# Kernel tuning notes

Hardware: AMD Instinct MI355X
Metric: run time of the kernel (lower is better)

Reference implementation:

```python
import jax, jax.numpy as jnp
import numpy as np

B, L, C = 16, 4096, 32
D = 512
W = 24                  # rolling window
LAGS = [3, 5, 7]
MAXLEN = 5000
EPS = 1e-5


def setup_inputs() -> dict:
    key = jax.random.key(0)
    ks = jax.random.split(key, 8)
    return {
        "x": jax.random.normal(ks[0], (B, L, C), jnp.float32),
        "conv_w": jax.random.normal(ks[1], (D, C * (5 + len(LAGS)), 3), jnp.float32) * 0.05,
        "conv_b": jnp.zeros((D,), jnp.float32),
        "learned_pe": jax.random.normal(ks[2], (1, MAXLEN, D), jnp.float32) * (1.0 / np.sqrt(D)),
        "tape_pos": jax.random.normal(ks[3], (MAXLEN, D), jnp.float32) * 0.02,
        "tproj_w": jax.random.normal(ks[4], (D, D), jnp.float32) * 0.02,
        "tproj_b": jnp.zeros((D,), jnp.float32),
        "mixer_w": jax.random.normal(ks[5], (D, 2 * D), jnp.float32) * 0.02,
        "mixer_b": jnp.zeros((D,), jnp.float32),
        "g_c": jnp.ones((D,), jnp.float32), "b_c": jnp.zeros((D,), jnp.float32),
        "g_f": jnp.ones((D,), jnp.float32), "b_f": jnp.zeros((D,), jnp.float32),
        "g_l": jnp.ones((D,), jnp.float32), "b_l": jnp.zeros((D,), jnp.float32),
        "g_t": jnp.ones((D,), jnp.float32), "b_t": jnp.zeros((D,), jnp.float32),
        "weight_params": jnp.array([0.25, 0.25, 0.25, 0.25], jnp.float32),
    }


def _layer_norm(h, g, b):
    m = jnp.mean(h, axis=-1, keepdims=True)
    v = jnp.mean((h - m) ** 2, axis=-1, keepdims=True)
    return g * (h - m) / jnp.sqrt(v + EPS) + b


def reference(x, conv_w, conv_b, learned_pe, tape_pos, tproj_w, tproj_b,
              mixer_w, mixer_b, g_c, b_c, g_f, b_f, g_l, b_l, g_t, b_t,
              weight_params):
    Bx, Lx, Cx = x.shape
    # --- RollingFeatureExtractor: replicate-pad left, sliding mean/max/min/std
    xp = jnp.pad(x, ((0, 0), (W - 1, 0), (0, 0)), mode="edge")          # [B, L+W-1, C]
    win = jnp.stack([xp[:, i:i + Lx, :] for i in range(W)], axis=2)       # [B, L, W, C]
    w_mean = jnp.mean(win, axis=2)
    w_max = jnp.max(win, axis=2)
    w_min = jnp.min(win, axis=2)
    w_var = jnp.sum((win - w_mean[:, :, None, :]) ** 2, axis=2) / (W - 1)  # unbiased, torch.std default
    w_std = jnp.sqrt(w_var)
    x_stats = jnp.concatenate([x, w_mean, w_max, w_min, w_std], axis=-1)  # [B, L, 5C]
    # --- lag differences (replicate pad left by max lag)
    ml = max(LAGS)
    xl = jnp.pad(x, ((0, 0), (ml, 0), (0, 0)), mode="edge")
    x_lags = jnp.concatenate([x - xl[:, ml - l:ml - l + Lx, :] for l in LAGS], axis=-1)  # [B, L, 3C]
    comb = jnp.concatenate([x_stats, x_lags], axis=-1)                    # [B, L, 8C]
    # --- TokenEmbedding: Conv1d k=3, circular padding
    h = comb.transpose(0, 2, 1)                                           # [B, 8C, L]
    h = jnp.pad(h, ((0, 0), (0, 0), (1, 1)), mode="wrap")
    h = jax.lax.conv_general_dilated(h, conv_w, (1,), "VALID",
                                     dimension_numbers=("NCH", "OIH", "NCH"))
    h = h + conv_b[None, :, None]
    combined_emb = _layer_norm(h.transpose(0, 2, 1), g_c, b_c)            # [B, L, D]
    # --- fixed sinusoidal PE (constant / detached)
    pos = jnp.arange(Lx)
    div = jnp.exp(jnp.arange(0, D, 2).astype(x.dtype) * (-(np.log(10000.0) / D)))
    ang = pos[:, None].astype(x.dtype) * div[None, :]                     # [L, D/2]
    pe_fixed_tab = jnp.zeros((Lx, D), x.dtype).at[:, 0::2].set(jnp.sin(ang)).at[:, 1::2].set(jnp.cos(ang))
    pe_fixed = _layer_norm(pe_fixed_tab, g_f, b_f)[None]                  # [1, L, D]
    # --- learnable PE
    pe_learned = _layer_norm(learned_pe[:, :Lx], g_l, b_l)                # [1, L, D]
    # --- tAPE: token proj + learned pos embedding -> mixer linear
    pe = tape_pos[pos]                                                    # [L, D]
    tok = combined_emb @ tproj_w.T + tproj_b                              # [B, L, D]
    mixed = jnp.concatenate([tok, jnp.broadcast_to(pe[None], tok.shape)], axis=-1)
    pe_tape = _layer_norm(mixed @ mixer_w.T + mixer_b, g_t, b_t)          # [B, L, D]
    # --- softmax-weighted sum (dropout is identity in eval)
    w = jax.nn.softmax(weight_params)
    return (w[0] * combined_emb + w[1] * pe_fixed + w[2] * pe_learned + w[3] * pe_tape)
```

## Files before the change

### kernel.cpp

```cpp
#include <hip/hip_runtime.h>
#include <stdint.h>


typedef unsigned short u16;
using short8  = __attribute__((ext_vector_type(8))) short;
using floatx4 = __attribute__((ext_vector_type(4))) float;
typedef __attribute__((address_space(1))) const unsigned int u32_as1;
typedef __attribute__((address_space(3))) unsigned int       u32_as3;

static __device__ __forceinline__ u16 f2b(float f) {
  unsigned u = __float_as_uint(f);
  u += 0x7FFFu + ((u >> 16) & 1u);
  return (u16)(u >> 16);
}
static __device__ __forceinline__ float b2f(u16 h) {
  return __uint_as_float(((unsigned)h) << 16);
}

__global__ __launch_bounds__(256) void prep_mats(
    const float* __restrict__ conv_w, const float* __restrict__ mixer_w,
    const float* __restrict__ tproj_w, const float* __restrict__ tape_pos,
    u16* __restrict__ W1, u16* __restrict__ A_m1, u16* __restrict__ M2t,
    u16* __restrict__ tprojT, u16* __restrict__ tape_bf) {
  int i = blockIdx.x * 256 + threadIdx.x;
  if (i < 393216) {
    int d = i / 768, rem = i - d * 768;
    int j = rem >> 8, c = rem & 255;
    W1[i] = f2b(conv_w[(d * 256 + c) * 3 + j]);
  } else if (i < 393216 + 262144) {
    int k = i - 393216; int p = k >> 9, r = k & 511;
    A_m1[k] = f2b(mixer_w[p * 1024 + r]);
  } else if (i < 393216 + 524288) {
    int k = i - 393216 - 262144; int p = k >> 9, r = k & 511;
    M2t[k] = f2b(mixer_w[p * 1024 + 512 + r]);
  } else if (i < 393216 + 786432) {
    int k = i - 393216 - 524288; int q = k >> 9, r = k & 511;
    tprojT[k] = f2b(tproj_w[r * 512 + q]);
  } else if (i < 393216 + 786432 + 2097152) {
    int k = i - 393216 - 786432;
    tape_bf[k] = f2b(tape_pos[k]);
  }
}

__global__ __launch_bounds__(256) void bias2_k(
    const float* __restrict__ mixer_w, const float* __restrict__ tproj_b,
    const float* __restrict__ mixer_b, float* __restrict__ bias2) {
  int p = blockIdx.x * 256 + threadIdx.x;
  if (p < 512) {
    float s = mixer_b[p];
    for (int r = 0; r < 512; ++r) s += mixer_w[p * 1024 + r] * tproj_b[r];
    bias2[p] = s;
  }
}

__global__ __launch_bounds__(256) void feat_kernel(
    const float* __restrict__ x, u16* __restrict__ comb) {
  __shared__ float sx[87 * 32];
  const int b = blockIdx.y, l0 = blockIdx.x * 64;
  for (int idx = threadIdx.x; idx < 87 * 32; idx += 256) {
    int r = idx >> 5, c = idx & 31;
    int ls = l0 - 23 + r; if (ls < 0) ls = 0;
    sx[idx] = x[((size_t)b * 4096 + ls) * 32 + c];
  }
  __syncthreads();
  const int c = threadIdx.x & 31, lr0 = threadIdx.x >> 5;
  for (int pass = 0; pass < 8; ++pass) {
    int lr = pass * 8 + lr0;
    int l = l0 + lr;
    float w[24];
    float s = 0.f, mx = -3.4e38f, mn = 3.4e38f;
    #pragma unroll
    for (int i = 0; i < 24; ++i) {
      float v = sx[(lr + i) * 32 + c];
      w[i] = v; s += v; mx = fmaxf(mx, v); mn = fminf(mn, v);
    }
    float mean = s * (1.f / 24.f);
    float ssd = 0.f;
    #pragma unroll
    for (int i = 0; i < 24; ++i) { float d = w[i] - mean; ssd += d * d; }
    float sd = sqrtf(fmaxf(ssd, 0.f) * (1.f / 23.f));
    float xv = w[23];
    float lag3 = xv - sx[(lr + 20) * 32 + c];
    float lag5 = xv - sx[(lr + 18) * 32 + c];
    float lag7 = xv - sx[(lr + 16) * 32 + c];
    size_t base = ((size_t)b * 4096 + l) * 256 + c;
    comb[base +   0] = f2b(xv);
    comb[base +  32] = f2b(mean);
    comb[base +  64] = f2b(mx);
    comb[base +  96] = f2b(mn);
    comb[base + 128] = f2b(sd);
    comb[base + 160] = f2b(lag3);
    comb[base + 192] = f2b(lag5);
    comb[base + 224] = f2b(lag7);
  }
}

__global__ __launch_bounds__(256) void gemm_bt(
    const u16* __restrict__ A, const u16* __restrict__ Bt,
    void* __restrict__ outp, int K, int ldc,
    const float* __restrict__ bias, int outBf16) {
  __shared__ __align__(16) u16 lA[128 * 64];
  __shared__ __align__(16) u16 lB[128 * 64];
  const int tid = threadIdx.x;
  const int m0 = blockIdx.x * 128, n0 = blockIdx.y * 128;
  const int wave = tid >> 6, lane = tid & 63;
  const int wm = (wave & 1) * 64, wn = (wave >> 1) * 64;
  const int quad = lane >> 4, r16 = lane & 15;
  const int rowT = tid >> 3, col8 = tid & 7;

  floatx4 acc[4][4];
  #pragma unroll
  for (int i = 0; i < 4; ++i)
    #pragma unroll
    for (int j = 0; j < 4; ++j) acc[i][j] = (floatx4){0.f, 0.f, 0.f, 0.f};

  for (int kk = 0; kk < K; kk += 64) {
    __syncthreads();
    #pragma unroll
    for (int it = 0; it < 4; ++it) {
      int rr = it * 32 + rowT;
      const u16* ga = A  + (size_t)(m0 + rr) * K + kk + col8 * 8;
      const u16* gb = Bt + (size_t)(n0 + rr) * K + kk + col8 * 8;
      __builtin_amdgcn_global_load_lds((u32_as1*)ga, (u32_as3*)&lA[rr * 64 + col8 * 8], 16, 0, 0);
      __builtin_amdgcn_global_load_lds((u32_as1*)gb, (u32_as3*)&lB[rr * 64 + col8 * 8], 16, 0, 0);
    }
    __syncthreads();
    #pragma unroll
    for (int ks = 0; ks < 64; ks += 32) {
      short8 af[4], bfr[4];
      #pragma unroll
      for (int i = 0; i < 4; ++i)
        af[i] = *(const short8*)&lA[(wm + i * 16 + r16) * 64 + ks + quad * 8];
      #pragma unroll
      for (int j = 0; j < 4; ++j)
        bfr[j] = *(const short8*)&lB[(wn + j * 16 + r16) * 64 + ks + quad * 8];
      #pragma unroll
      for (int i = 0; i < 4; ++i)
        #pragma unroll
        for (int j = 0; j < 4; ++j)
          acc[i][j] = __builtin_amdgcn_mfma_f32_16x16x32_bf16(af[i], bfr[j], acc[i][j], 0, 0, 0);
    }
  }
  #pragma unroll
  for (int i = 0; i < 4; ++i) {
    #pragma unroll
    for (int rr = 0; rr < 4; ++rr) {
      int m = m0 + wm + i * 16 + quad * 4 + rr;
      #pragma unroll
      for (int j = 0; j < 4; ++j) {
        int n = n0 + wn + j * 16 + r16;
        float v = acc[i][j][rr];
        if (bias) v += bias[n];
        if (outBf16) ((u16*)outp)[(size_t)m * ldc + n] = f2b(v);
        else         ((float*)outp)[(size_t)m * ldc + n] = v;
      }
    }
  }
}


#define STAGE_A(SRCEXPR)                                                       \
  _Pragma("unroll")                                                            \
  for (int it = 0; it < 2; ++it) {                                             \
    int id = it * 256 + tid, row = id >> 3, c = id & 7;                        \
    int cg = ((c ^ (row & 7)) << 3);                                           \
    const u16* gsrc = (SRCEXPR);                                               \
    __builtin_amdgcn_global_load_lds((u32_as1*)gsrc,                           \
        (u32_as3*)(smem + id * 16), 16, 0, 0);                                 \
  }
#define STAGE_B(SRCEXPR)                                                       \
  _Pragma("unroll")                                                            \
  for (int it = 0; it < 16; ++it) {                                            \
    int id = it * 256 + tid, row = id >> 3, c = id & 7;                        \
    int cg = ((c ^ (row & 7)) << 3);                                           \
    const u16* gsrc = (SRCEXPR);                                               \
    __builtin_amdgcn_global_load_lds((u32_as1*)gsrc,                           \
        (u32_as3*)(smem + 8192 + id * 16), 16, 0, 0);                          \
  }

__global__ __launch_bounds__(256, 2) void gemm_conv_ln(
    const u16* __restrict__ comb, const u16* __restrict__ W1,
    const float* __restrict__ conv_b, const float* __restrict__ g_c,
    const float* __restrict__ b_c, u16* __restrict__ ce) {
  __shared__ __align__(16) char smem[73728];
  __shared__ float sG[512], sB[512], sBias[512];
  u16* lA = (u16*)smem;
  u16* lB = (u16*)(smem + 8192);
  u16* lT = (u16*)smem;

  const int tid = threadIdx.x;
  if (tid < 128) {
    ((float4*)sG)[tid]    = ((const float4*)g_c)[tid];
    ((float4*)sB)[tid]    = ((const float4*)b_c)[tid];
    ((float4*)sBias)[tid] = ((const float4*)conv_b)[tid];
  }
  const int m0 = blockIdx.x * 64;
  const int b = m0 >> 12, l0 = m0 & 4095;
  const int w = tid >> 6, lane = tid & 63;
  const int quad = lane >> 4, r16 = lane & 15;

  floatx4 acc[4][8];
  #pragma unroll
  for (int i = 0; i < 4; ++i)
    #pragma unroll
    for (int jj = 0; jj < 8; ++jj) acc[i][jj] = (floatx4){0.f, 0.f, 0.f, 0.f};

  for (int kk = 0; kk < 768; kk += 64) {
    const int jsh = kk >> 8, kc = kk & 255;
    __syncthreads();
    STAGE_A(comb + (((size_t)b * 4096 + ((l0 + row + jsh - 1 + 4096) & 4095)) << 8) + kc + cg)
    STAGE_B(W1 + (size_t)row * 768 + kk + cg)
    __syncthreads();
    #pragma unroll
    for (int ks = 0; ks < 64; ks += 32) {
      short8 af[4];
      #pragma unroll
      for (int i = 0; i < 4; ++i) {
        int row = i * 16 + r16;
        af[i] = *(const short8*)&lA[row * 64 + ((((ks >> 3) + quad) ^ (row & 7)) << 3)];
      }
      #pragma unroll
      for (int jj = 0; jj < 8; ++jj) {
        int row = w * 128 + jj * 16 + r16;
        short8 bf = *(const short8*)&lB[row * 64 + ((((ks >> 3) + quad) ^ (row & 7)) << 3)];
        #pragma unroll
        for (int i = 0; i < 4; ++i)
          acc[i][jj] = __builtin_amdgcn_mfma_f32_16x16x32_bf16(bf, af[i], acc[i][jj], 0, 0, 0);
      }
    }
  }
  __syncthreads();
  #pragma unroll
  for (int jj = 0; jj < 8; ++jj) {
    int n = w * 128 + jj * 16 + quad * 4;
    float4 b4 = *(const float4*)&sBias[n];
    #pragma unroll
    for (int i = 0; i < 4; ++i) {
      ushort4 pk;
      pk.x = f2b(acc[i][jj][0] + b4.x);
      pk.y = f2b(acc[i][jj][1] + b4.y);
      pk.z = f2b(acc[i][jj][2] + b4.z);
      pk.w = f2b(acc[i][jj][3] + b4.w);
      *(ushort4*)(lT + (size_t)(i * 16 + r16) * 520 + n) = pk;
    }
  }
  __syncthreads();
  const int orow = tid >> 2, part = tid & 3;
  const u16* rowp = lT + (size_t)orow * 520;
  float s1 = 0.f, s2 = 0.f;
  #pragma unroll
  for (int k = 0; k < 16; ++k) {
    short8 t8 = *(const short8*)(rowp + (part + k * 4) * 8);
    #pragma unroll
    for (int e = 0; e < 8; ++e) {
      float f = b2f((u16)t8[e]); s1 += f; s2 += f * f;
    }
  }
  s1 += __shfl_xor(s1, 1); s2 += __shfl_xor(s2, 1);
  s1 += __shfl_xor(s1, 2); s2 += __shfl_xor(s2, 2);
  float mean = s1 * (1.f / 512.f);
  float inv = rsqrtf(fmaxf(s2 * (1.f / 512.f) - mean * mean, 0.f) + 1e-5f);
  size_t mrow = (size_t)(m0 + orow) * 512;
  #pragma unroll
  for (int k = 0; k < 16; ++k) {
    int c8 = part + k * 4;
    short8 t8 = *(const short8*)(rowp + c8 * 8);
    short8 o;
    #pragma unroll
    for (int e = 0; e < 8; ++e) {
      int d = c8 * 8 + e;
      o[e] = (short)f2b(sG[d] * ((b2f((u16)t8[e]) - mean) * inv) + sB[d]);
    }
    *(short8*)(ce + mrow + c8 * 8) = o;
  }
}

__global__ __launch_bounds__(256, 2) void gemm_pre_final(
    const u16* __restrict__ ceA, const u16* __restrict__ Wf,
    const u16* __restrict__ ctab_bf, const u16* __restrict__ pf_tab,
    const u16* __restrict__ pl_tab, const float* __restrict__ g_t,
    const float* __restrict__ b_t, const float* __restrict__ wp,
    float* __restrict__ out) {
  __shared__ __align__(16) char smem[73728];
  __shared__ float sG[512], sB[512];
  u16* lA = (u16*)smem;
  u16* lB = (u16*)(smem + 8192);
  u16* lT = (u16*)smem;

  const int tid = threadIdx.x;
  if (tid < 128) {
    ((float4*)sG)[tid] = ((const float4*)g_t)[tid];
    ((float4*)sB)[tid] = ((const float4*)b_t)[tid];
  }
  const int m0 = blockIdx.x * 64;
  const int l0m = m0 & 4095;
  const int w = tid >> 6, lane = tid & 63;
  const int quad = lane >> 4, r16 = lane & 15;

  floatx4 acc[4][8];
  #pragma unroll
  for (int i = 0; i < 4; ++i)
    #pragma unroll
    for (int jj = 0; jj < 8; ++jj) acc[i][jj] = (floatx4){0.f, 0.f, 0.f, 0.f};

  for (int kk = 0; kk < 512; kk += 64) {
    __syncthreads();
    STAGE_A(ceA + (size_t)(m0 + row) * 512 + kk + cg)
    STAGE_B(Wf + (size_t)row * 512 + kk + cg)
    __syncthreads();
    #pragma unroll
    for (int ks = 0; ks < 64; ks += 32) {
      short8 af[4];
      #pragma unroll
      for (int i = 0; i < 4; ++i) {
        int row = i * 16 + r16;
        af[i] = *(const short8*)&lA[row * 64 + ((((ks >> 3) + quad) ^ (row & 7)) << 3)];
      }
      #pragma unroll
      for (int jj = 0; jj < 8; ++jj) {
        int row = w * 128 + jj * 16 + r16;
        short8 bf = *(const short8*)&lB[row * 64 + ((((ks >> 3) + quad) ^ (row & 7)) << 3)];
        #pragma unroll
        for (int i = 0; i < 4; ++i)
          acc[i][jj] = __builtin_amdgcn_mfma_f32_16x16x32_bf16(bf, af[i], acc[i][jj], 0, 0, 0);
      }
    }
  }
  __syncthreads();
  #pragma unroll
  for (int jj = 0; jj < 8; ++jj) {
    int n = w * 128 + jj * 16 + quad * 4;
    #pragma unroll
    for (int i = 0; i < 4; ++i) {
      ushort4 pk;
      pk.x = f2b(acc[i][jj][0]);
      pk.y = f2b(acc[i][jj][1]);
      pk.z = f2b(acc[i][jj][2]);
      pk.w = f2b(acc[i][jj][3]);
      *(ushort4*)(lT + (size_t)(i * 16 + r16) * 520 + n) = pk;
    }
  }
  __syncthreads();
  const int orow = tid >> 2, part = tid & 3;
  const int m = m0 + orow, l = l0m + orow;
  const u16* rowp = lT + (size_t)orow * 520;
  const size_t lrow = (size_t)l * 512, mrow = (size_t)m * 512;
  float s1 = 0.f, s2 = 0.f;
  #pragma unroll
  for (int k = 0; k < 16; ++k) {
    int c8 = part + k * 4;
    short8 t8 = *(const short8*)(rowp + c8 * 8);
    short8 ct = *(const short8*)(ctab_bf + lrow + c8 * 8);
    #pragma unroll
    for (int e = 0; e < 8; ++e) {
      float f = b2f((u16)t8[e]) + b2f((u16)ct[e]);
      s1 += f; s2 += f * f;
    }
  }
  s1 += __shfl_xor(s1, 1); s2 += __shfl_xor(s2, 1);
  s1 += __shfl_xor(s1, 2); s2 += __shfl_xor(s2, 2);
  float mean = s1 * (1.f / 512.f);
  float inv = rsqrtf(fmaxf(s2 * (1.f / 512.f) - mean * mean, 0.f) + 1e-5f);

  float a0 = wp[0], a1 = wp[1], a2 = wp[2], a3 = wp[3];
  float mxw = fmaxf(fmaxf(a0, a1), fmaxf(a2, a3));
  float e0 = expf(a0 - mxw), e1 = expf(a1 - mxw), e2 = expf(a2 - mxw), e3 = expf(a3 - mxw);
  float invs = 1.f / (e0 + e1 + e2 + e3);
  float w0 = e0 * invs, w1 = e1 * invs, w2 = e2 * invs, w3 = e3 * invs;

  #pragma unroll
  for (int k = 0; k < 16; ++k) {
    int c8 = part + k * 4;
    short8 t8  = *(const short8*)(rowp + c8 * 8);
    short8 ct  = *(const short8*)(ctab_bf + lrow + c8 * 8);
    short8 c8v = *(const short8*)(ceA + mrow + c8 * 8);
    short8 pf  = *(const short8*)(pf_tab + lrow + c8 * 8);
    short8 pl  = *(const short8*)(pl_tab + lrow + c8 * 8);
    float o[8];
    #pragma unroll
    for (int e = 0; e < 8; ++e) {
      int d = c8 * 8 + e;
      float f = b2f((u16)t8[e]) + b2f((u16)ct[e]);
      float pt = sG[d] * ((f - mean) * inv) + sB[d];
      o[e] = w0 * b2f((u16)c8v[e]) + w1 * b2f((u16)pf[e]) + w2 * b2f((u16)pl[e]) + w3 * pt;
    }
    float4* op = (float4*)(out + mrow + c8 * 8);
    op[0] = make_float4(o[0], o[1], o[2], o[3]);
    op[1] = make_float4(o[4], o[5], o[6], o[7]);
  }
}

__global__ __launch_bounds__(256) void pe_tables(
    const float* __restrict__ learned_pe,
    const float* __restrict__ gf, const float* __restrict__ bf_,
    const float* __restrict__ gl, const float* __restrict__ bl,
    u16* __restrict__ pf_tab, u16* __restrict__ pl_tab) {
  int row = blockIdx.x * 4 + (threadIdx.x >> 6);
  int lane = threadIdx.x & 63;
  size_t base = (size_t)row * 512 + lane * 8;
  float v[8]; float s1 = 0.f, s2 = 0.f;
  #pragma unroll
  for (int e = 0; e < 8; ++e) {
    int d = lane * 8 + e;
    int de = d & ~1;
    float div = expf((float)de * (-9.210340371976184f / 512.f));
    float ang = (float)row * div;
    v[e] = (d & 1) ? cosf(ang) : sinf(ang);
    s1 += v[e]; s2 += v[e] * v[e];
  }
  #pragma unroll
  for (int off = 32; off; off >>= 1) { s1 += __shfl_xor(s1, off); s2 += __shfl_xor(s2, off); }
  float mean = s1 * (1.f / 512.f);
  float inv = rsqrtf(fmaxf(s2 * (1.f / 512.f) - mean * mean, 0.f) + 1e-5f);
  short8 o;
  #pragma unroll
  for (int e = 0; e < 8; ++e) {
    int d = lane * 8 + e;
    o[e] = (short)f2b(gf[d] * ((v[e] - mean) * inv) + bf_[d]);
  }
  *(short8*)(pf_tab + base) = o;
  const float4* lp = (const float4*)(learned_pe + base);
  float4 a = lp[0], bq = lp[1];
  float u[8] = {a.x, a.y, a.z, a.w, bq.x, bq.y, bq.z, bq.w};
  s1 = 0.f; s2 = 0.f;
  #pragma unroll
  for (int e = 0; e < 8; ++e) { s1 += u[e]; s2 += u[e] * u[e]; }
  #pragma unroll
  for (int off = 32; off; off >>= 1) { s1 += __shfl_xor(s1, off); s2 += __shfl_xor(s2, off); }
  mean = s1 * (1.f / 512.f);
  inv = rsqrtf(fmaxf(s2 * (1.f / 512.f) - mean * mean, 0.f) + 1e-5f);
  #pragma unroll
  for (int e = 0; e < 8; ++e) {
    int d = lane * 8 + e;
    o[e] = (short)f2b(gl[d] * ((u[e] - mean) * inv) + bl[d]);
  }
  *(short8*)(pl_tab + base) = o;
}

extern "C" void kernel_launch(void* const* d_in, const int* in_sizes, int n_in,
                              void* d_out, int out_size, void* d_ws, size_t ws_size,
                              hipStream_t stream) {
  const float* x          = (const float*)d_in[0];
  const float* conv_w     = (const float*)d_in[1];
  const float* conv_b     = (const float*)d_in[2];
  const float* learned_pe = (const float*)d_in[3];
  const float* tape_pos   = (const float*)d_in[4];
  const float* tproj_w    = (const float*)d_in[5];
  const float* tproj_b    = (const float*)d_in[6];
  const float* mixer_w    = (const float*)d_in[7];
  const float* mixer_b    = (const float*)d_in[8];
  const float* g_c        = (const float*)d_in[9];
  const float* b_c        = (const float*)d_in[10];
  const float* g_f        = (const float*)d_in[11];
  const float* b_f        = (const float*)d_in[12];
  const float* g_l        = (const float*)d_in[13];
  const float* b_l        = (const float*)d_in[14];
  const float* g_t        = (const float*)d_in[15];
  const float* b_t        = (const float*)d_in[16];
  const float* wp         = (const float*)d_in[17];

  char* ws = (char*)d_ws;
  u16*  comb    = (u16*)(ws + 0);
  u16*  ce      = (u16*)(ws + 33554432);
  char* S       = ws + 100663296;
  u16*  W1      = (u16*)(S + 0);
  u16*  A_m1    = (u16*)(S + 786432);
  u16*  M2t     = (u16*)(S + 1310720);
  u16*  tprojT  = (u16*)(S + 1835008);
  u16*  tape_bf = (u16*)(S + 2359296);
  u16*  Wf      = (u16*)(S + 6553600);
  u16*  ctab_bf = (u16*)(S + 7077888);
  float* bias2  = (float*)(S + 11272192);
  u16*  pf_tab  = (u16*)(S + 11274240);
  u16*  pl_tab  = (u16*)(S + 15468544);

  prep_mats<<<12800, 256, 0, stream>>>(conv_w, mixer_w, tproj_w, tape_pos,
                                       W1, A_m1, M2t, tprojT, tape_bf);
  bias2_k<<<2, 256, 0, stream>>>(mixer_w, tproj_b, mixer_b, bias2);
  feat_kernel<<<dim3(64, 16), 256, 0, stream>>>(x, comb);
  gemm_bt<<<dim3(4, 4), 256, 0, stream>>>(A_m1, tprojT, Wf, 512, 512, nullptr, 1);
  gemm_bt<<<dim3(32, 4), 256, 0, stream>>>(tape_bf, M2t, ctab_bf, 512, 512, bias2, 1);
  pe_tables<<<1024, 256, 0, stream>>>(learned_pe, g_f, b_f, g_l, b_l, pf_tab, pl_tab);
  gemm_conv_ln<<<1024, 256, 0, stream>>>(comb, W1, conv_b, g_c, b_c, ce);
  gemm_pre_final<<<1024, 256, 0, stream>>>(ce, Wf, ctab_bf, pf_tab, pl_tab,
                                           g_t, b_t, wp, (float*)d_out);
}
```

Before: 390.8 us.

## Double-buffer A tiles, read B weights from global, merge prep kernels

The two large GEMM kernels now double-buffer the activation tile in LDS, prefetching the next K slice while the current one is computed. Weight fragments are read straight from global memory (L2-resident) into registers instead of being staged through LDS, and the MFMA sections are wrapped with s_setprio. The prep, bias and PE-table kernels are merged into one launch to cut launch overhead. The risk is higher global-load latency on the B operand and more register pressure.

```diff
diff --git a/kernel.cpp b/kernel.cpp
--- a/kernel.cpp
+++ b/kernel.cpp
@@ -17,40 +17,88 @@
   return __uint_as_float(((unsigned)h) << 16);
 }
 
-__global__ __launch_bounds__(256) void prep_mats(
+__global__ __launch_bounds__(256) void prep_all(
     const float* __restrict__ conv_w, const float* __restrict__ mixer_w,
     const float* __restrict__ tproj_w, const float* __restrict__ tape_pos,
+    const float* __restrict__ tproj_b, const float* __restrict__ mixer_b,
+    const float* __restrict__ learned_pe,
+    const float* __restrict__ gf, const float* __restrict__ bf_,
+    const float* __restrict__ gl, const float* __restrict__ bl,
     u16* __restrict__ W1, u16* __restrict__ A_m1, u16* __restrict__ M2t,
-    u16* __restrict__ tprojT, u16* __restrict__ tape_bf) {
-  int i = blockIdx.x * 256 + threadIdx.x;
-  if (i < 393216) {
-    int d = i / 768, rem = i - d * 768;
-    int j = rem >> 8, c = rem & 255;
-    W1[i] = f2b(conv_w[(d * 256 + c) * 3 + j]);
-  } else if (i < 393216 + 262144) {
-    int k = i - 393216; int p = k >> 9, r = k & 511;
-    A_m1[k] = f2b(mixer_w[p * 1024 + r]);
-  } else if (i < 393216 + 524288) {
-    int k = i - 393216 - 262144; int p = k >> 9, r = k & 511;
-    M2t[k] = f2b(mixer_w[p * 1024 + 512 + r]);
-  } else if (i < 393216 + 786432) {
-    int k = i - 393216 - 524288; int q = k >> 9, r = k & 511;
-    tprojT[k] = f2b(tproj_w[r * 512 + q]);
-  } else if (i < 393216 + 786432 + 2097152) {
-    int k = i - 393216 - 786432;
-    tape_bf[k] = f2b(tape_pos[k]);
-  }
-}
-
-__global__ __launch_bounds__(256) void bias2_k(
-    const float* __restrict__ mixer_w, const float* __restrict__ tproj_b,
-    const float* __restrict__ mixer_b, float* __restrict__ bias2) {
-  int p = blockIdx.x * 256 + threadIdx.x;
-  if (p < 512) {
-    float s = mixer_b[p];
-    for (int r = 0; r < 512; ++r) s += mixer_w[p * 1024 + r] * tproj_b[r];
-    bias2[p] = s;
-  }
+    u16* __restrict__ tprojT, u16* __restrict__ tape_bf,
+    float* __restrict__ bias2, u16* __restrict__ pf_tab,
+    u16* __restrict__ pl_tab) {
+  const int bx = blockIdx.x;
+  if (bx < 12800) {
+    int i = bx * 256 + threadIdx.x;
+    if (i < 393216) {
+      int d = i / 768, rem = i - d * 768;
+      int j = rem >> 8, c = rem & 255;
+      W1[i] = f2b(conv_w[(d * 256 + c) * 3 + j]);
+    } else if (i < 393216 + 262144) {
+      int k = i - 393216; int p = k >> 9, r = k & 511;
+      A_m1[k] = f2b(mixer_w[p * 1024 + r]);
+    } else if (i < 393216 + 524288) {
+      int k = i - 393216 - 262144; int p = k >> 9, r = k & 511;
+      M2t[k] = f2b(mixer_w[p * 1024 + 512 + r]);
+    } else if (i < 393216 + 786432) {
+      int k = i - 393216 - 524288; int q = k >> 9, r = k & 511;
+      tprojT[k] = f2b(tproj_w[r * 512 + q]);
+    } else if (i < 393216 + 786432 + 2097152) {
+      int k = i - 393216 - 786432;
+      tape_bf[k] = f2b(tape_pos[k]);
+    }
+    return;
+  }
+  if (bx < 12802) {
+    int p = (bx - 12800) * 256 + threadIdx.x;
+    if (p < 512) {
+      float s = mixer_b[p];
+      for (int r = 0; r < 512; ++r) s += mixer_w[p * 1024 + r] * tproj_b[r];
+      bias2[p] = s;
+    }
+    return;
+  }
+  int row = (bx - 12802) * 4 + (threadIdx.x >> 6);
+  int lane = threadIdx.x & 63;
+  size_t base = (size_t)row * 512 + lane * 8;
+  float v[8]; float s1 = 0.f, s2 = 0.f;
+  #pragma unroll
+  for (int e = 0; e < 8; ++e) {
+    int d = lane * 8 + e;
+    int de = d & ~1;
+    float div = expf((float)de * (-9.210340371976184f / 512.f));
+    float ang = (float)row * div;
+    v[e] = (d & 1) ? cosf(ang) : sinf(ang);
+    s1 += v[e]; s2 += v[e] * v[e];
+  }
+  #pragma unroll
+  for (int off = 32; off; off >>= 1) { s1 += __shfl_xor(s1, off); s2 += __shfl_xor(s2, off); }
+  float mean = s1 * (1.f / 512.f);
+  float inv = rsqrtf(fmaxf(s2 * (1.f / 512.f) - mean * mean, 0.f) + 1e-5f);
+  short8 o;
+  #pragma unroll
+  for (int e = 0; e < 8; ++e) {
+    int d = lane * 8 + e;
+    o[e] = (short)f2b(gf[d] * ((v[e] - mean) * inv) + bf_[d]);
+  }
+  *(short8*)(pf_tab + base) = o;
+  const float4* lp = (const float4*)(learned_pe + base);
+  float4 a = lp[0], bq = lp[1];
+  float u[8] = {a.x, a.y, a.z, a.w, bq.x, bq.y, bq.z, bq.w};
+  s1 = 0.f; s2 = 0.f;
+  #pragma unroll
+  for (int e = 0; e < 8; ++e) { s1 += u[e]; s2 += u[e] * u[e]; }
+  #pragma unroll
+  for (int off = 32; off; off >>= 1) { s1 += __shfl_xor(s1, off); s2 += __shfl_xor(s2, off); }
+  mean = s1 * (1.f / 512.f);
+  inv = rsqrtf(fmaxf(s2 * (1.f / 512.f) - mean * mean, 0.f) + 1e-5f);
+  #pragma unroll
+  for (int e = 0; e < 8; ++e) {
+    int d = lane * 8 + e;
+    o[e] = (short)f2b(gl[d] * ((u[e] - mean) * inv) + bl[d]);
+  }
+  *(short8*)(pl_tab + base) = o;
 }
 
 __global__ __launch_bounds__(256) void feat_kernel(
@@ -159,33 +207,22 @@
 }
 
 
-#define STAGE_A(SRCEXPR)                                                       \
+#define STAGE_A(BUFOFF, SRCEXPR)                                               \
   _Pragma("unroll")                                                            \
   for (int it = 0; it < 2; ++it) {                                             \
     int id = it * 256 + tid, row = id >> 3, c = id & 7;                        \
-    int cg = ((c ^ (row & 7)) << 3);                                           \
+    int cg = ((c ^ (row & 7)) << 3); (void)cg;                                 \
     const u16* gsrc = (SRCEXPR);                                               \
     __builtin_amdgcn_global_load_lds((u32_as1*)gsrc,                           \
-        (u32_as3*)(smem + id * 16), 16, 0, 0);                                 \
-  }
-#define STAGE_B(SRCEXPR)                                                       \
-  _Pragma("unroll")                                                            \
-  for (int it = 0; it < 16; ++it) {                                            \
-    int id = it * 256 + tid, row = id >> 3, c = id & 7;                        \
-    int cg = ((c ^ (row & 7)) << 3);                                           \
-    const u16* gsrc = (SRCEXPR);                                               \
-    __builtin_amdgcn_global_load_lds((u32_as1*)gsrc,                           \
-        (u32_as3*)(smem + 8192 + id * 16), 16, 0, 0);                          \
+        (u32_as3*)(smem + (BUFOFF) + id * 16), 16, 0, 0);                      \
   }
 
 __global__ __launch_bounds__(256, 2) void gemm_conv_ln(
     const u16* __restrict__ comb, const u16* __restrict__ W1,
     const float* __restrict__ conv_b, const float* __restrict__ g_c,
     const float* __restrict__ b_c, u16* __restrict__ ce) {
-  __shared__ __align__(16) char smem[73728];
+  __shared__ __align__(16) char smem[66560];
   __shared__ float sG[512], sB[512], sBias[512];
-  u16* lA = (u16*)smem;
-  u16* lB = (u16*)(smem + 8192);
   u16* lT = (u16*)smem;
 
   const int tid = threadIdx.x;
@@ -198,6 +235,8 @@
   const int b = m0 >> 12, l0 = m0 & 4095;
   const int w = tid >> 6, lane = tid & 63;
   const int quad = lane >> 4, r16 = lane & 15;
+  const int wn = w * 128;
+  const u16* bw = W1 + (size_t)(wn + r16) * 768 + quad * 8;
 
   floatx4 acc[4][8];
   #pragma unroll
@@ -205,34 +244,43 @@
     #pragma unroll
     for (int jj = 0; jj < 8; ++jj) acc[i][jj] = (floatx4){0.f, 0.f, 0.f, 0.f};
 
-  for (int kk = 0; kk < 768; kk += 64) {
-    const int jsh = kk >> 8, kc = kk & 255;
-    __syncthreads();
-    STAGE_A(comb + (((size_t)b * 4096 + ((l0 + row + jsh - 1 + 4096) & 4095)) << 8) + kc + cg)
-    STAGE_B(W1 + (size_t)row * 768 + kk + cg)
-    __syncthreads();
-    #pragma unroll
-    for (int ks = 0; ks < 64; ks += 32) {
-      short8 af[4];
+  STAGE_A(0, comb + (((size_t)b * 4096 + ((l0 + row - 1 + 4096) & 4095)) << 8) + cg)
+  __syncthreads();
+
+  for (int t = 0; t < 12; ++t) {
+    const int kk = t * 64;
+    const u16* lAc = (const u16*)(smem + (t & 1) * 8192);
+    if (t + 1 < 12) {
+      const int kk2 = kk + 64;
+      const int jsh = kk2 >> 8, kc = kk2 & 255;
+      STAGE_A((1 - (t & 1)) * 8192,
+          comb + (((size_t)b * 4096 + ((l0 + row + jsh - 1 + 4096) & 4095)) << 8) + kc + cg)
+    }
+    #pragma unroll
+    for (int s = 0; s < 2; ++s) {
+      short8 bf[8], af[4];
+      #pragma unroll
+      for (int jj = 0; jj < 8; ++jj)
+        bf[jj] = *(const short8*)(bw + (size_t)jj * 12288 + kk + s * 32);
       #pragma unroll
       for (int i = 0; i < 4; ++i) {
         int row = i * 16 + r16;
-        af[i] = *(const short8*)&lA[row * 64 + ((((ks >> 3) + quad) ^ (row & 7)) << 3)];
+        af[i] = *(const short8*)((const u16*)lAc + row * 64 + (((s * 4 + quad) ^ (row & 7)) << 3));
       }
-      #pragma unroll
-      for (int jj = 0; jj < 8; ++jj) {
-        int row = w * 128 + jj * 16 + r16;
-        short8 bf = *(const short8*)&lB[row * 64 + ((((ks >> 3) + quad) ^ (row & 7)) << 3)];
+      __builtin_amdgcn_s_setprio(1);
+      #pragma unroll
+      for (int jj = 0; jj < 8; ++jj)
         #pragma unroll
         for (int i = 0; i < 4; ++i)
-          acc[i][jj] = __builtin_amdgcn_mfma_f32_16x16x32_bf16(bf, af[i], acc[i][jj], 0, 0, 0);
-      }
-    }
-  }
-  __syncthreads();
+          acc[i][jj] = __builtin_amdgcn_mfma_f32_16x16x32_bf16(bf[jj], af[i], acc[i][jj], 0, 0, 0);
+      __builtin_amdgcn_s_setprio(0);
+    }
+    __syncthreads();
+  }
+
   #pragma unroll
   for (int jj = 0; jj < 8; ++jj) {
-    int n = w * 128 + jj * 16 + quad * 4;
+    int n = wn + jj * 16 + quad * 4;
     float4 b4 = *(const float4*)&sBias[n];
     #pragma unroll
     for (int i = 0; i < 4; ++i) {
@@ -281,10 +329,8 @@
     const u16* __restrict__ pl_tab, const float* __restrict__ g_t,
     const float* __restrict__ b_t, const float* __restrict__ wp,
     float* __restrict__ out) {
-  __shared__ __align__(16) char smem[73728];
+  __shared__ __align__(16) char smem[66560];
   __shared__ float sG[512], sB[512];
-  u16* lA = (u16*)smem;
-  u16* lB = (u16*)(smem + 8192);
   u16* lT = (u16*)smem;
 
   const int tid = threadIdx.x;
@@ -296,6 +342,8 @@
   const int l0m = m0 & 4095;
   const int w = tid >> 6, lane = tid & 63;
   const int quad = lane >> 4, r16 = lane & 15;
+  const int wn = w * 128;
+  const u16* bw = Wf + (size_t)(wn + r16) * 512 + quad * 8;
 
   floatx4 acc[4][8];
   #pragma unroll
@@ -303,33 +351,41 @@
     #pragma unroll
     for (int jj = 0; jj < 8; ++jj) acc[i][jj] = (floatx4){0.f, 0.f, 0.f, 0.f};
 
-  for (int kk = 0; kk < 512; kk += 64) {
-    __syncthreads();
-    STAGE_A(ceA + (size_t)(m0 + row) * 512 + kk + cg)
-    STAGE_B(Wf + (size_t)row * 512 + kk + cg)
-    __syncthreads();
-    #pragma unroll
-    for (int ks = 0; ks < 64; ks += 32) {
-      short8 af[4];
+  STAGE_A(0, ceA + (size_t)(m0 + row) * 512 + cg)
+  __syncthreads();
+
+  for (int t = 0; t < 8; ++t) {
+    const int kk = t * 64;
+    const u16* lAc = (const u16*)(smem + (t & 1) * 8192);
+    if (t + 1 < 8) {
+      STAGE_A((1 - (t & 1)) * 8192,
+          ceA + (size_t)(m0 + row) * 512 + kk + 64 + cg)
+    }
+    #pragma unroll
+    for (int s = 0; s < 2; ++s) {
+      short8 bf[8], af[4];
+      #pragma unroll
+      for (int jj = 0; jj < 8; ++jj)
+        bf[jj] = *(const short8*)(bw + (size_t)jj * 8192 + kk + s * 32);
       #pragma unroll
       for (int i = 0; i < 4; ++i) {
         int row = i * 16 + r16;
-        af[i] = *(const short8*)&lA[row * 64 + ((((ks >> 3) + quad) ^ (row & 7)) << 3)];
+        af[i] = *(const short8*)((const u16*)lAc + row * 64 + (((s * 4 + quad) ^ (row & 7)) << 3));
       }
-      #pragma unroll
-      for (int jj = 0; jj < 8; ++jj) {
-        int row = w * 128 + jj * 16 + r16;
-        short8 bf = *(const short8*)&lB[row * 64 + ((((ks >> 3) + quad) ^ (row & 7)) << 3)];
+      __builtin_amdgcn_s_setprio(1);
+      #pragma unroll
+      for (int jj = 0; jj < 8; ++jj)
         #pragma unroll
         for (int i = 0; i < 4; ++i)
-          acc[i][jj] = __builtin_amdgcn_mfma_f32_16x16x32_bf16(bf, af[i], acc[i][jj], 0, 0, 0);
-      }
-    }
-  }
-  __syncthreads();
+          acc[i][jj] = __builtin_amdgcn_mfma_f32_16x16x32_bf16(bf[jj], af[i], acc[i][jj], 0, 0, 0);
+      __builtin_amdgcn_s_setprio(0);
+    }
+    __syncthreads();
+  }
+
   #pragma unroll
   for (int jj = 0; jj < 8; ++jj) {
-    int n = w * 128 + jj * 16 + quad * 4;
+    int n = wn + jj * 16 + quad * 4;
     #pragma unroll
     for (int i = 0; i < 4; ++i) {
       ushort4 pk;
@@ -388,53 +444,6 @@
     op[0] = make_float4(o[0], o[1], o[2], o[3]);
     op[1] = make_float4(o[4], o[5], o[6], o[7]);
   }
-}
-
-__global__ __launch_bounds__(256) void pe_tables(
-    const float* __restrict__ learned_pe,
-    const float* __restrict__ gf, const float* __restrict__ bf_,
-    const float* __restrict__ gl, const float* __restrict__ bl,
-    u16* __restrict__ pf_tab, u16* __restrict__ pl_tab) {
-  int row = blockIdx.x * 4 + (threadIdx.x >> 6);
-  int lane = threadIdx.x & 63;
-  size_t base = (size_t)row * 512 + lane * 8;
-  float v[8]; float s1 = 0.f, s2 = 0.f;
-  #pragma unroll
-  for (int e = 0; e < 8; ++e) {
-    int d = lane * 8 + e;
-    int de = d & ~1;
-    float div = expf((float)de * (-9.210340371976184f / 512.f));
-    float ang = (float)row * div;
-    v[e] = (d & 1) ? cosf(ang) : sinf(ang);
-    s1 += v[e]; s2 += v[e] * v[e];
-  }
-  #pragma unroll
-  for (int off = 32; off; off >>= 1) { s1 += __shfl_xor(s1, off); s2 += __shfl_xor(s2, off); }
-  float mean = s1 * (1.f / 512.f);
-  float inv = rsqrtf(fmaxf(s2 * (1.f / 512.f) - mean * mean, 0.f) + 1e-5f);
-  short8 o;
-  #pragma unroll
-  for (int e = 0; e < 8; ++e) {
-    int d = lane * 8 + e;
-    o[e] = (short)f2b(gf[d] * ((v[e] - mean) * inv) + bf_[d]);
-  }
-  *(short8*)(pf_tab + base) = o;
-  const float4* lp = (const float4*)(learned_pe + base);
-  float4 a = lp[0], bq = lp[1];
-  float u[8] = {a.x, a.y, a.z, a.w, bq.x, bq.y, bq.z, bq.w};
-  s1 = 0.f; s2 = 0.f;
-  #pragma unroll
-  for (int e = 0; e < 8; ++e) { s1 += u[e]; s2 += u[e] * u[e]; }
-  #pragma unroll
-  for (int off = 32; off; off >>= 1) { s1 += __shfl_xor(s1, off); s2 += __shfl_xor(s2, off); }
-  mean = s1 * (1.f / 512.f);
-  inv = rsqrtf(fmaxf(s2 * (1.f / 512.f) - mean * mean, 0.f) + 1e-5f);
-  #pragma unroll
-  for (int e = 0; e < 8; ++e) {
-    int d = lane * 8 + e;
-    o[e] = (short)f2b(gl[d] * ((u[e] - mean) * inv) + bl[d]);
-  }
-  *(short8*)(pl_tab + base) = o;
 }
 
 extern "C" void kernel_launch(void* const* d_in, const int* in_sizes, int n_in,
@@ -474,13 +483,14 @@
   u16*  pf_tab  = (u16*)(S + 11274240);
   u16*  pl_tab  = (u16*)(S + 15468544);
 
-  prep_mats<<<12800, 256, 0, stream>>>(conv_w, mixer_w, tproj_w, tape_pos,
-                                       W1, A_m1, M2t, tprojT, tape_bf);
-  bias2_k<<<2, 256, 0, stream>>>(mixer_w, tproj_b, mixer_b, bias2);
+  prep_all<<<13826, 256, 0, stream>>>(conv_w, mixer_w, tproj_w, tape_pos,
+                                      tproj_b, mixer_b, learned_pe,
+                                      g_f, b_f, g_l, b_l,
+                                      W1, A_m1, M2t, tprojT, tape_bf,
+                                      bias2, pf_tab, pl_tab);
   feat_kernel<<<dim3(64, 16), 256, 0, stream>>>(x, comb);
   gemm_bt<<<dim3(4, 4), 256, 0, stream>>>(A_m1, tprojT, Wf, 512, 512, nullptr, 1);
   gemm_bt<<<dim3(32, 4), 256, 0, stream>>>(tape_bf, M2t, ctab_bf, 512, 512, bias2, 1);
-  pe_tables<<<1024, 256, 0, stream>>>(learned_pe, g_f, b_f, g_l, b_l, pf_tab, pl_tab);
   gemm_conv_ln<<<1024, 256, 0, stream>>>(comb, W1, conv_b, g_c, b_c, ce);
   gemm_pre_final<<<1024, 256, 0, stream>>>(ce, Wf, ctab_bf, pf_tab, pl_tab,
                                            g_t, b_t, wp, (float*)d_out);
```

New measurement: 447.4 us. 1.14x slower.
